# Kernel tuning notes

Hardware: AMD Instinct MI355X
Metric: run time of the kernel (lower is better)

Reference implementation:

```python
import jax, jax.numpy as jnp
import numpy as np

B, H, W, C = 32, 56, 56, 384
HEADS, WIN, SHIFT = 12, 7, 3
MLP_HID = 4 * C
N = WIN * WIN
EPS = 1e-5


def _rel_pos_index(win):
    ch, cw = np.meshgrid(np.arange(win), np.arange(win), indexing='ij')
    coords = np.stack([ch.ravel(), cw.ravel()])            # (2, N)
    rel = coords[:, :, None] - coords[:, None, :]          # (2, N, N)
    rel = rel.transpose(1, 2, 0).astype(np.int64)
    rel[:, :, 0] += win - 1
    rel[:, :, 1] += win - 1
    rel[:, :, 0] *= 2 * win - 1
    return rel.sum(-1)                                     # (N, N)


def _attn_mask(Hh, Ww, win, shift):
    img = np.zeros((Hh, Ww))
    cnt = 0
    slices = (slice(0, -win), slice(-win, -shift), slice(-shift, None))
    for hs in slices:
        for ws in slices:
            img[hs, ws] = cnt
            cnt += 1
    m = img.reshape(Hh // win, win, Ww // win, win).transpose(0, 2, 1, 3).reshape(-1, win * win)
    am = m[:, None, :] - m[:, :, None]
    return np.where(am != 0, -100.0, 0.0).astype(np.float32)  # (nW, N, N)


REL_IDX = jnp.asarray(_rel_pos_index(WIN))
ATTN_MASK = jnp.asarray(_attn_mask(H, W, WIN, SHIFT))


def setup_inputs() -> dict:
    key = jax.random.key(0)
    ks = jax.random.split(key, 16)
    s = 0.02
    return {
        'x': jax.random.normal(ks[0], (B, H * W, C), jnp.float32),
        'g1': jnp.ones((C,), jnp.float32),
        'b1': jnp.zeros((C,), jnp.float32),
        'qkv_w': jax.random.normal(ks[1], (3 * C, C), jnp.float32) * s,
        'qkv_b': jnp.zeros((3 * C,), jnp.float32),
        'rel_bias': jax.random.normal(ks[2], ((2 * WIN - 1) ** 2, HEADS), jnp.float32) * s,
        'proj_w': jax.random.normal(ks[3], (C, C), jnp.float32) * s,
        'proj_b': jnp.zeros((C,), jnp.float32),
        'g2': jnp.ones((C,), jnp.float32),
        'b2': jnp.zeros((C,), jnp.float32),
        'fc1_w': jax.random.normal(ks[4], (MLP_HID, C), jnp.float32) * s,
        'fc1_b': jnp.zeros((MLP_HID,), jnp.float32),
        'fc2_w': jax.random.normal(ks[5], (C, MLP_HID), jnp.float32) * s,
        'fc2_b': jnp.zeros((C,), jnp.float32),
    }


def _ln(x, g, b):
    m = x.mean(-1, keepdims=True)
    v = jnp.var(x, axis=-1, keepdims=True)
    return (x - m) * jax.lax.rsqrt(v + EPS) * g + b


def reference(x, g1, b1, qkv_w, qkv_b, rel_bias, proj_w, proj_b, g2, b2, fc1_w, fc1_b, fc2_w, fc2_b):
    Bz, L, Cc = x.shape
    hd = Cc // HEADS
    nWh = H // WIN
    shortcut = x

    h = _ln(x, g1, b1).reshape(Bz, H, W, Cc)
    h = jnp.roll(h, (-SHIFT, -SHIFT), axis=(1, 2))
    # window partition -> (Bz*nW, N, C)
    h = h.reshape(Bz, nWh, WIN, nWh, WIN, Cc).transpose(0, 1, 3, 2, 4, 5).reshape(-1, N, Cc)

    qkv = (h @ qkv_w.T + qkv_b).reshape(-1, N, 3, HEADS, hd).transpose(2, 0, 3, 1, 4)
    q, k, v = qkv[0] * (hd ** -0.5), qkv[1], qkv[2]
    attn = jnp.einsum('bhnd,bhmd->bhnm', q, k)  # (Bz*nW, heads, N, N)

    bias = rel_bias[REL_IDX.reshape(-1)].reshape(N, N, HEADS).transpose(2, 0, 1)
    attn = attn + bias[None]

    nW = ATTN_MASK.shape[0]
    attn = attn.reshape(Bz, nW, HEADS, N, N) + ATTN_MASK[None, :, None]
    attn = jax.nn.softmax(attn, axis=-1).reshape(-1, HEADS, N, N)

    out = jnp.einsum('bhnm,bhmd->bhnd', attn, v).transpose(0, 2, 1, 3).reshape(-1, N, Cc)
    out = out @ proj_w.T + proj_b
    # window reverse + unshift
    out = out.reshape(Bz, nWh, nWh, WIN, WIN, Cc).transpose(0, 1, 3, 2, 4, 5).reshape(Bz, H, W, Cc)
    out = jnp.roll(out, (SHIFT, SHIFT), axis=(1, 2)).reshape(Bz, L, Cc)

    x = shortcut + out
    h2 = _ln(x, g2, b2)
    h2 = jax.nn.gelu(h2 @ fc1_w.T + fc1_b, approximate=False)
    h2 = h2 @ fc2_w.T + fc2_b
    return x + h2
```

## Files before the change

kernel.cpp:

```cpp
#include <hip/hip_runtime.h>
#include <hip/hip_bf16.h>
#include <math.h>

#define B_      32
#define H_      56
#define W_      56
#define C_      384
#define HEADS_  12
#define WIN_    7
#define SHIFT_  3
#define NTOK_   49
#define HD_     32
#define T_      100352
#define MLP_    1536
#define TCH_    50176

typedef __bf16 bf16x8 __attribute__((ext_vector_type(8)));
typedef unsigned short u16x8 __attribute__((ext_vector_type(8)));
typedef float  f32x4  __attribute__((ext_vector_type(4)));

__device__ __forceinline__ float bf2f(unsigned short u) {
  union { unsigned int i; float f; } v; v.i = ((unsigned int)u) << 16; return v.f;
}
__device__ __forceinline__ unsigned short f2bf(float f) {
  union { float f; unsigned int i; } v; v.f = f;
  unsigned int x = v.i;
  return (unsigned short)((x + 0x7fffu + ((x >> 16) & 1u)) >> 16);
}
__device__ __forceinline__ float gelu_fast(float x) {
  const float t = 0.79788456f * x * (1.0f + 0.044715f * x * x);
  const float e = __expf(2.0f * t);
  const float th = 1.0f - 2.0f / (e + 1.0f);
  return 0.5f * x * (1.0f + th);
}
__device__ __forceinline__ void gload_lds16(const void* g, void* l) {
  __builtin_amdgcn_global_load_lds(
      (const __attribute__((address_space(1))) void*)g,
      (__attribute__((address_space(3))) void*)l, 16, 0, 0);
}
__device__ __forceinline__ bf16x8 ldg8(const unsigned short* p) {
  u16x8 v = *(const u16x8*)p;
  return __builtin_bit_cast(bf16x8, v);
}

__global__ __launch_bounds__(256)
void wconv_all_kernel(const float* __restrict__ s0, unsigned short* __restrict__ d0,
                      const float* __restrict__ s1, unsigned short* __restrict__ d1,
                      const float* __restrict__ s2, unsigned short* __restrict__ d2,
                      const float* __restrict__ s3, unsigned short* __restrict__ d3) {
  int b = blockIdx.x;
  const float* src; unsigned short* dst;
  if (b < 432)       { src = s0; dst = d0; }
  else if (b < 576)  { src = s1; dst = d1; b -= 432; }
  else if (b < 1152) { src = s2; dst = d2; b -= 576; }
  else               { src = s3; dst = d3; b -= 1152; }
  const int i = (b * 256 + threadIdx.x) * 4;
  const float4 v = *(const float4*)(src + i);
  ushort4 o;
  o.x = f2bf(v.x); o.y = f2bf(v.y); o.z = f2bf(v.z); o.w = f2bf(v.w);
  *(ushort4*)(dst + i) = o;
}

template<int REMAP>
__global__ __launch_bounds__(256)
void ln_kernel(const float* __restrict__ xin, const float* __restrict__ g,
               const float* __restrict__ bb, unsigned short* __restrict__ outbf) {
  const int m = blockIdx.x * 4 + (threadIdx.x >> 6);
  const int lane = threadIdx.x & 63;
  size_t src;
  if (REMAP) {
    int w = m / NTOK_, t = m - w * NTOK_;
    int bz = w >> 6, widx = w & 63;
    int wh = widx >> 3, ww = widx & 7;
    int ih = t / WIN_, iw = t - ih * WIN_;
    int gh = (wh * WIN_ + ih + SHIFT_) % H_;
    int gw = (ww * WIN_ + iw + SHIFT_) % W_;
    src = ((size_t)bz * (H_ * W_) + gh * W_ + gw) * C_;
  } else {
    src = (size_t)m * C_;
  }
  const float2* row2 = (const float2*)(xin + src);
  float2 v[3]; float s = 0.f, s2 = 0.f;
#pragma unroll
  for (int u = 0; u < 3; ++u) {
    v[u] = row2[lane + 64 * u];
    s  += v[u].x + v[u].y;
    s2 += v[u].x * v[u].x + v[u].y * v[u].y;
  }
#pragma unroll
  for (int off = 32; off; off >>= 1) {
    s  += __shfl_xor(s, off);
    s2 += __shfl_xor(s2, off);
  }
  const float mean = s * (1.0f / C_);
  const float var  = s2 * (1.0f / C_) - mean * mean;
  const float rstd = rsqrtf(var + 1e-5f);
  unsigned short* orow = outbf + (size_t)m * C_;
#pragma unroll
  for (int u = 0; u < 3; ++u) {
    const int c = (lane + 64 * u) * 2;
    ushort2 o;
    o.x = f2bf((v[u].x - mean) * rstd * g[c]     + bb[c]);
    o.y = f2bf((v[u].y - mean) * rstd * g[c + 1] + bb[c + 1]);
    *(ushort2*)(orow + c) = o;
  }
}

#define BM 256
#define BN 128
#define BKg 64

template<int EPI>
__global__ __launch_bounds__(512)
void mfma_gemm(const unsigned short* __restrict__ A,
               const unsigned short* __restrict__ Wb,
               const float* __restrict__ bias,
               void* __restrict__ outv,
               const float* __restrict__ resid,
               int M, int Nn, int K) {
  __shared__ unsigned short Al[BM * BKg];
  __shared__ unsigned short Bl[BN * BKg];
  const int t    = threadIdx.x;
  const int wid  = t >> 6;
  const int lane = t & 63;
  const int wr   = wid >> 1, wc = wid & 1;

  const unsigned int nb = gridDim.x * gridDim.y;
  const unsigned int lin = blockIdx.y * gridDim.x + blockIdx.x;
  const unsigned int q = nb >> 3, r = nb & 7;
  const unsigned int xcd = lin & 7, idx = lin >> 3;
  const unsigned int wg = (xcd < r ? xcd * (q + 1) : r * (q + 1) + (xcd - r) * q) + idx;
  const int m0 = (int)(wg / gridDim.x) * BM;
  const int n0 = (int)(wg % gridDim.x) * BN;

  f32x4 acc[4][4] = {};

  const int sr8    = lane >> 3;
  const int schunk = (lane & 7) ^ (sr8 & 7);
  const int fr  = lane & 15;
  const int fq  = lane >> 4;

  for (int k0 = 0; k0 < K; k0 += BKg) {
    __syncthreads();
#pragma unroll
    for (int i = 0; i < 4; ++i) {
      const int rr = i * 64 + wid * 8 + sr8;
      gload_lds16(A + (size_t)(m0 + rr) * K + k0 + schunk * 8,
                  (void*)(Al + (size_t)(i * 64 + wid * 8) * BKg));
    }
#pragma unroll
    for (int i = 0; i < 2; ++i) {
      const int rr = i * 64 + wid * 8 + sr8;
      gload_lds16(Wb + (size_t)(n0 + rr) * K + k0 + schunk * 8,
                  (void*)(Bl + (size_t)(i * 64 + wid * 8) * BKg));
    }
    __syncthreads();

#pragma unroll
    for (int kk = 0; kk < 2; ++kk) {
      bf16x8 af[4], bfr[4];
#pragma unroll
      for (int mi = 0; mi < 4; ++mi) {
        const int row = wr * 64 + mi * 16 + fr;
        const int ch  = (kk * 4 + fq) ^ (row & 7);
        af[mi] = *(const bf16x8*)(Al + (size_t)row * BKg + ch * 8);
      }
#pragma unroll
      for (int ni = 0; ni < 4; ++ni) {
        const int row = wc * 64 + ni * 16 + fr;
        const int ch  = (kk * 4 + fq) ^ (row & 7);
        bfr[ni] = *(const bf16x8*)(Bl + (size_t)row * BKg + ch * 8);
      }
#pragma unroll
      for (int mi = 0; mi < 4; ++mi)
#pragma unroll
        for (int ni = 0; ni < 4; ++ni)
          acc[mi][ni] = __builtin_amdgcn_mfma_f32_16x16x32_bf16(
              af[mi], bfr[ni], acc[mi][ni], 0, 0, 0);
    }
  }

  const int ecol  = fr;
  const int erow0 = fq * 4;
#pragma unroll
  for (int mi = 0; mi < 4; ++mi) {
#pragma unroll
    for (int r2 = 0; r2 < 4; ++r2) {
      const int m = m0 + wr * 64 + mi * 16 + erow0 + r2;
      size_t dstbase = 0;
      if (EPI == 2) {
        int w = m / NTOK_, tt = m - w * NTOK_;
        int bz = w >> 6, widx = w & 63;
        int wh = widx >> 3, ww = widx & 7;
        int ih = tt / WIN_, iw = tt - ih * WIN_;
        int gh = (wh * WIN_ + ih + SHIFT_) % H_;
        int gw = (ww * WIN_ + iw + SHIFT_) % W_;
        dstbase = ((size_t)bz * (H_ * W_) + gh * W_ + gw) * C_;
      }
#pragma unroll
      for (int ni = 0; ni < 4; ++ni) {
        const int n = n0 + wc * 64 + ni * 16 + ecol;
        float val = acc[mi][ni][r2] + bias[n];
        if (EPI == 0) {
          ((unsigned short*)outv)[(size_t)m * Nn + n] = f2bf(val);
        } else if (EPI == 1) {
          ((unsigned short*)outv)[(size_t)m * Nn + n] = f2bf(gelu_fast(val));
        } else if (EPI == 2) {
          ((float*)outv)[dstbase + n] = resid[dstbase + n] + val;
        } else {
          float* o = (float*)outv + (size_t)m * Nn + n;
          *o += val;
        }
      }
    }
  }
}

__global__ __launch_bounds__(64)
void bias_expand_kernel(const float* __restrict__ rel_bias,
                        float* __restrict__ biasx) {
  const int hi = blockIdx.x;
  const int head = hi / NTOK_, i = hi - head * NTOK_;
  const int j = threadIdx.x;
  float v = 0.f;
  if (j < NTOK_) {
    const int ih = i / 7, iw = i - ih * 7;
    const int jh = j / 7, jw = j - jh * 7;
    const int ridx = (ih - jh + 6) * 13 + (iw - jw + 6);
    v = rel_bias[ridx * HEADS_ + head];
  }
  biasx[(size_t)hi * 64 + j] = v;
}

#define AW 2
__global__ __launch_bounds__(64 * AW)
void attn_mfma_kernel(const unsigned short* __restrict__ qkv,
                      const float* __restrict__ biasx,
                      unsigned short* __restrict__ out) {
  __shared__ unsigned short sP[AW][64 * 72];
  __shared__ unsigned short sVT[AW][32 * 72];
  __shared__ float sRI[AW][64];
  const int wid  = threadIdx.x >> 6;
  const int lane = threadIdx.x & 63;
  const int task = blockIdx.x * AW + wid;
  const int w    = task / HEADS_;
  const int head = task - w * HEADS_;
  const int widx = w & 63;
  const int wh = widx >> 3, ww = widx & 7;
  const bool edge = (wh == 7) || (ww == 7);
  const int c  = lane & 15;
  const int fq = lane >> 4;
  unsigned short* Pl = sP[wid];
  unsigned short* Vl = sVT[wid];
  float* Ri = sRI[wid];
  const unsigned short* qw = qkv + (size_t)w * NTOK_ * (3 * C_);

  u16x8 vv[4];
#pragma unroll
  for (int p = 0; p < 4; ++p)
    vv[p] = *(const u16x8*)(qw + (size_t)(p * 16 + c) * (3 * C_) + 2 * C_ + head * HD_ + fq * 8);

  bf16x8 kf[4], qf[4];
#pragma unroll
  for (int nj = 0; nj < 4; ++nj)
    kf[nj] = ldg8(qw + (size_t)(nj * 16 + c) * (3 * C_) + C_ + head * HD_ + fq * 8);
#pragma unroll
  for (int qi = 0; qi < 4; ++qi)
    qf[qi] = ldg8(qw + (size_t)(qi * 16 + c) * (3 * C_) + head * HD_ + fq * 8);

  const f32x4 zero4 = {0.f, 0.f, 0.f, 0.f};
  f32x4 accT[4][4];
#pragma unroll
  for (int nj = 0; nj < 4; ++nj)
#pragma unroll
    for (int qi = 0; qi < 4; ++qi)
      accT[nj][qi] = __builtin_amdgcn_mfma_f32_16x16x32_bf16(kf[nj], qf[qi], zero4, 0, 0, 0);

#pragma unroll
  for (int p = 0; p < 4; ++p)
#pragma unroll
    for (int u = 0; u < 8; ++u)
      Vl[(fq * 8 + u) * 72 + p * 16 + c] = (unsigned short)vv[p][u];

  int lj16[16];
  unsigned jpad = 0;
#pragma unroll
  for (int tt = 0; tt < 16; ++tt) {
    const int j = (tt >> 2) * 16 + fq * 4 + (tt & 3);
    int lj = 0;
    if (j >= NTOK_) jpad |= (1u << tt);
    else if (edge) {
      const int jh = j / 7, jw2 = j - jh * 7;
      const int shj = wh * 7 + jh, swj = ww * 7 + jw2;
      lj = (shj < 49 ? 0 : (shj < 53 ? 1 : 2)) * 3 + (swj < 49 ? 0 : (swj < 53 ? 1 : 2));
    }
    lj16[tt] = lj;
  }

  const float* bh = biasx + (size_t)head * (NTOK_ * 64);
#pragma unroll
  for (int qi = 0; qi < 4; ++qi) {
    const int i  = qi * 16 + c;
    const int ic = i < NTOK_ ? i : 0;
    int li = 0;
    if (edge) {
      const int ih = ic / 7, iw2 = ic - ih * 7;
      const int shi = wh * 7 + ih, swi = ww * 7 + iw2;
      li = (shi < 49 ? 0 : (shi < 53 ? 1 : 2)) * 3 + (swi < 49 ? 0 : (swi < 53 ? 1 : 2));
    }
    float sv[16];
#pragma unroll
    for (int nj = 0; nj < 4; ++nj) {
      const float4 b4 = *(const float4*)(bh + ic * 64 + nj * 16 + fq * 4);
      const float* b4p = (const float*)&b4;
#pragma unroll
      for (int r = 0; r < 4; ++r) {
        const int tt = nj * 4 + r;
        float s = accT[nj][qi][r] * 0.17677669529663687f + b4p[r];
        if (edge && lj16[tt] != li) s -= 100.f;
        if (jpad & (1u << tt)) s = -1e30f;
        sv[tt] = s;
      }
    }
    float mx = sv[0];
#pragma unroll
    for (int tt = 1; tt < 16; ++tt) mx = fmaxf(mx, sv[tt]);
    mx = fmaxf(mx, __shfl_xor(mx, 16));
    mx = fmaxf(mx, __shfl_xor(mx, 32));
    float e[16]; float sm = 0.f;
#pragma unroll
    for (int tt = 0; tt < 16; ++tt) { e[tt] = __expf(sv[tt] - mx); sm += e[tt]; }
    sm += __shfl_xor(sm, 16);
    sm += __shfl_xor(sm, 32);
    if (fq == 0) Ri[i] = 1.0f / sm;
#pragma unroll
    for (int nj = 0; nj < 4; ++nj) {
      ushort4 pk;
      pk.x = f2bf(e[nj * 4 + 0]); pk.y = f2bf(e[nj * 4 + 1]);
      pk.z = f2bf(e[nj * 4 + 2]); pk.w = f2bf(e[nj * 4 + 3]);
      *(ushort4*)(Pl + (size_t)i * 72 + nj * 16 + fq * 4) = pk;
    }
  }

  f32x4 accO[4][2] = {};
#pragma unroll
  for (int kk = 0; kk < 2; ++kk) {
    bf16x8 ap[4], bv[2];
#pragma unroll
    for (int mi = 0; mi < 4; ++mi)
      ap[mi] = __builtin_bit_cast(bf16x8,
          *(const u16x8*)(Pl + (mi * 16 + c) * 72 + kk * 32 + fq * 8));
#pragma unroll
    for (int nd = 0; nd < 2; ++nd)
      bv[nd] = __builtin_bit_cast(bf16x8,
          *(const u16x8*)(Vl + (nd * 16 + c) * 72 + kk * 32 + fq * 8));
#pragma unroll
    for (int mi = 0; mi < 4; ++mi)
#pragma unroll
      for (int nd = 0; nd < 2; ++nd)
        accO[mi][nd] = __builtin_amdgcn_mfma_f32_16x16x32_bf16(ap[mi], bv[nd], accO[mi][nd], 0, 0, 0);
  }

#pragma unroll
  for (int mi = 0; mi < 4; ++mi)
#pragma unroll
    for (int r = 0; r < 4; ++r) {
      const int i = mi * 16 + fq * 4 + r;
      if (i < NTOK_) {
        const float inv = Ri[i];
#pragma unroll
        for (int nd = 0; nd < 2; ++nd)
          out[(size_t)(w * NTOK_ + i) * C_ + head * HD_ + nd * 16 + c] =
              f2bf(accO[mi][nd][r] * inv);
      }
    }
}

extern "C" void kernel_launch(void* const* d_in, const int* in_sizes, int n_in,
                              void* d_out, int out_size, void* d_ws, size_t ws_size,
                              hipStream_t stream) {
  const float* x        = (const float*)d_in[0];
  const float* g1       = (const float*)d_in[1];
  const float* b1       = (const float*)d_in[2];
  const float* qkv_w    = (const float*)d_in[3];
  const float* qkv_b    = (const float*)d_in[4];
  const float* rel_bias = (const float*)d_in[5];
  const float* proj_w   = (const float*)d_in[6];
  const float* proj_b   = (const float*)d_in[7];
  const float* g2       = (const float*)d_in[8];
  const float* b2       = (const float*)d_in[9];
  const float* fc1_w    = (const float*)d_in[10];
  const float* fc1_b    = (const float*)d_in[11];
  const float* fc2_w    = (const float*)d_in[12];
  const float* fc2_b    = (const float*)d_in[13];
  float* out = (float*)d_out;

  char* ws = (char*)d_ws;
  unsigned short* xw   = (unsigned short*)(ws);
  unsigned short* qkvb = (unsigned short*)(ws + 77070336);
  unsigned short* attn_out = xw;
  unsigned short* h2   = xw;
  unsigned short* hidc = qkvb;
  unsigned short* qkv_wb  = (unsigned short*)(ws + 308412416);
  unsigned short* proj_wb = (unsigned short*)(ws + 309297152);
  unsigned short* fc1_wb  = (unsigned short*)(ws + 309592064);
  unsigned short* fc2_wb  = (unsigned short*)(ws + 310771712);
  float*          biasx   = (float*)(ws + 311951360);

  wconv_all_kernel<<<dim3(1728), dim3(256), 0, stream>>>(
      qkv_w, qkv_wb, proj_w, proj_wb, fc1_w, fc1_wb, fc2_w, fc2_wb);
  bias_expand_kernel<<<dim3(HEADS_ * NTOK_), dim3(64), 0, stream>>>(rel_bias, biasx);

  ln_kernel<1><<<dim3(T_ / 4), dim3(256), 0, stream>>>(x, g1, b1, xw);

  mfma_gemm<0><<<dim3(1152 / BN, T_ / BM), dim3(512), 0, stream>>>(
      xw, qkv_wb, qkv_b, (void*)qkvb, nullptr, T_, 1152, 384);

  attn_mfma_kernel<<<dim3((T_ / NTOK_) * HEADS_ / AW), dim3(64 * AW), 0, stream>>>(
      qkvb, biasx, attn_out);

  mfma_gemm<2><<<dim3(384 / BN, T_ / BM), dim3(512), 0, stream>>>(
      attn_out, proj_wb, proj_b, (void*)out, x, T_, 384, 384);

  ln_kernel<0><<<dim3(T_ / 4), dim3(256), 0, stream>>>(out, g2, b2, h2);

  for (int chk = 0; chk < 2; ++chk) {
    const size_t row0 = (size_t)chk * TCH_;
    mfma_gemm<1><<<dim3(MLP_ / BN, TCH_ / BM), dim3(512), 0, stream>>>(
        h2 + row0 * C_, fc1_wb, fc1_b, (void*)hidc, nullptr, TCH_, MLP_, 384);
    mfma_gemm<3><<<dim3(384 / BN, TCH_ / BM), dim3(512), 0, stream>>>(
        hidc, fc2_wb, fc2_b, (void*)(out + row0 * C_), nullptr, TCH_, 384, MLP_);
  }
}
```

Before: 891.5 us.

## Merge prologue kernels, swizzle V LDS layout, raise MFMA priority

After: 883.6 us. About the same (-0.9%).

```diff
diff --git a/kernel.cpp b/kernel.cpp
--- a/kernel.cpp
+++ b/kernel.cpp
@@ -44,42 +44,87 @@
 }
 
 __global__ __launch_bounds__(256)
-void wconv_all_kernel(const float* __restrict__ s0, unsigned short* __restrict__ d0,
-                      const float* __restrict__ s1, unsigned short* __restrict__ d1,
-                      const float* __restrict__ s2, unsigned short* __restrict__ d2,
-                      const float* __restrict__ s3, unsigned short* __restrict__ d3) {
+void prologue_kernel(const float* __restrict__ s0, unsigned short* __restrict__ d0,
+                     const float* __restrict__ s1, unsigned short* __restrict__ d1,
+                     const float* __restrict__ s2, unsigned short* __restrict__ d2,
+                     const float* __restrict__ s3, unsigned short* __restrict__ d3,
+                     const float* __restrict__ rel_bias, float* __restrict__ biasx,
+                     const float* __restrict__ x, const float* __restrict__ g1,
+                     const float* __restrict__ b1, unsigned short* __restrict__ xw) {
   int b = blockIdx.x;
-  const float* src; unsigned short* dst;
-  if (b < 432)       { src = s0; dst = d0; }
-  else if (b < 576)  { src = s1; dst = d1; b -= 432; }
-  else if (b < 1152) { src = s2; dst = d2; b -= 576; }
-  else               { src = s3; dst = d3; b -= 1152; }
-  const int i = (b * 256 + threadIdx.x) * 4;
-  const float4 v = *(const float4*)(src + i);
-  ushort4 o;
-  o.x = f2bf(v.x); o.y = f2bf(v.y); o.z = f2bf(v.z); o.w = f2bf(v.w);
-  *(ushort4*)(dst + i) = o;
-}
-
-template<int REMAP>
-__global__ __launch_bounds__(256)
-void ln_kernel(const float* __restrict__ xin, const float* __restrict__ g,
-               const float* __restrict__ bb, unsigned short* __restrict__ outbf) {
-  const int m = blockIdx.x * 4 + (threadIdx.x >> 6);
-  const int lane = threadIdx.x & 63;
-  size_t src;
-  if (REMAP) {
+  if (b < 1728) {
+    const float* src; unsigned short* dst;
+    if (b < 432)       { src = s0; dst = d0; }
+    else if (b < 576)  { src = s1; dst = d1; b -= 432; }
+    else if (b < 1152) { src = s2; dst = d2; b -= 576; }
+    else               { src = s3; dst = d3; b -= 1152; }
+    const int i = (b * 256 + threadIdx.x) * 4;
+    const float4 v = *(const float4*)(src + i);
+    ushort4 o;
+    o.x = f2bf(v.x); o.y = f2bf(v.y); o.z = f2bf(v.z); o.w = f2bf(v.w);
+    *(ushort4*)(dst + i) = o;
+    return;
+  }
+  if (b < 1875) {
+    const int hi = (b - 1728) * 4 + (threadIdx.x >> 6);
+    const int j = threadIdx.x & 63;
+    if (hi < HEADS_ * NTOK_) {
+      const int head = hi / NTOK_, i = hi - head * NTOK_;
+      float v = 0.f;
+      if (j < NTOK_) {
+        const int ih = i / 7, iw = i - ih * 7;
+        const int jh = j / 7, jw = j - jh * 7;
+        const int ridx = (ih - jh + 6) * 13 + (iw - jw + 6);
+        v = rel_bias[ridx * HEADS_ + head];
+      }
+      biasx[(size_t)hi * 64 + j] = v;
+    }
+    return;
+  }
+  {
+    const int m = (b - 1875) * 4 + (threadIdx.x >> 6);
+    const int lane = threadIdx.x & 63;
     int w = m / NTOK_, t = m - w * NTOK_;
     int bz = w >> 6, widx = w & 63;
     int wh = widx >> 3, ww = widx & 7;
     int ih = t / WIN_, iw = t - ih * WIN_;
     int gh = (wh * WIN_ + ih + SHIFT_) % H_;
     int gw = (ww * WIN_ + iw + SHIFT_) % W_;
-    src = ((size_t)bz * (H_ * W_) + gh * W_ + gw) * C_;
-  } else {
-    src = (size_t)m * C_;
-  }
-  const float2* row2 = (const float2*)(xin + src);
+    const size_t srcoff = ((size_t)bz * (H_ * W_) + gh * W_ + gw) * C_;
+    const float2* row2 = (const float2*)(x + srcoff);
+    float2 v[3]; float sa = 0.f, sb = 0.f;
+#pragma unroll
+    for (int u = 0; u < 3; ++u) {
+      v[u] = row2[lane + 64 * u];
+      sa += v[u].x + v[u].y;
+      sb += v[u].x * v[u].x + v[u].y * v[u].y;
+    }
+#pragma unroll
+    for (int off = 32; off; off >>= 1) {
+      sa += __shfl_xor(sa, off);
+      sb += __shfl_xor(sb, off);
+    }
+    const float mean = sa * (1.0f / C_);
+    const float var  = sb * (1.0f / C_) - mean * mean;
+    const float rstd = rsqrtf(var + 1e-5f);
+    unsigned short* orow = xw + (size_t)m * C_;
+#pragma unroll
+    for (int u = 0; u < 3; ++u) {
+      const int cc = (lane + 64 * u) * 2;
+      ushort2 o;
+      o.x = f2bf((v[u].x - mean) * rstd * g1[cc]     + b1[cc]);
+      o.y = f2bf((v[u].y - mean) * rstd * g1[cc + 1] + b1[cc + 1]);
+      *(ushort2*)(orow + cc) = o;
+    }
+  }
+}
+
+__global__ __launch_bounds__(256)
+void ln_kernel(const float* __restrict__ xin, const float* __restrict__ g,
+               const float* __restrict__ bb, unsigned short* __restrict__ outbf) {
+  const int m = blockIdx.x * 4 + (threadIdx.x >> 6);
+  const int lane = threadIdx.x & 63;
+  const float2* row2 = (const float2*)(xin + (size_t)m * C_);
   float2 v[3]; float s = 0.f, s2 = 0.f;
 #pragma unroll
   for (int u = 0; u < 3; ++u) {
@@ -214,22 +259,6 @@
       }
     }
   }
-}
-
-__global__ __launch_bounds__(64)
-void bias_expand_kernel(const float* __restrict__ rel_bias,
-                        float* __restrict__ biasx) {
-  const int hi = blockIdx.x;
-  const int head = hi / NTOK_, i = hi - head * NTOK_;
-  const int j = threadIdx.x;
-  float v = 0.f;
-  if (j < NTOK_) {
-    const int ih = i / 7, iw = i - ih * 7;
-    const int jh = j / 7, jw = j - jh * 7;
-    const int ridx = (ih - jh + 6) * 13 + (iw - jw + 6);
-    v = rel_bias[ridx * HEADS_ + head];
-  }
-  biasx[(size_t)hi * 64 + j] = v;
 }
 
 #define AW 2
@@ -270,17 +299,22 @@
 
   const f32x4 zero4 = {0.f, 0.f, 0.f, 0.f};
   f32x4 accT[4][4];
+  __builtin_amdgcn_s_setprio(1);
 #pragma unroll
   for (int nj = 0; nj < 4; ++nj)
 #pragma unroll
     for (int qi = 0; qi < 4; ++qi)
       accT[nj][qi] = __builtin_amdgcn_mfma_f32_16x16x32_bf16(kf[nj], qf[qi], zero4, 0, 0, 0);
+  __builtin_amdgcn_s_setprio(0);
 
 #pragma unroll
   for (int p = 0; p < 4; ++p)
 #pragma unroll
-    for (int u = 0; u < 8; ++u)
-      Vl[(fq * 8 + u) * 72 + p * 16 + c] = (unsigned short)vv[p][u];
+    for (int u = 0; u < 8; ++u) {
+      const int d  = fq * 8 + u;
+      const int ch = (2 * p + (c >> 3)) ^ ((u + fq) & 7);
+      Vl[d * 72 + ch * 8 + (c & 7)] = (unsigned short)vv[p][u];
+    }
 
   int lj16[16];
   unsigned jpad = 0;
@@ -351,14 +385,18 @@
       ap[mi] = __builtin_bit_cast(bf16x8,
           *(const u16x8*)(Pl + (mi * 16 + c) * 72 + kk * 32 + fq * 8));
 #pragma unroll
-    for (int nd = 0; nd < 2; ++nd)
-      bv[nd] = __builtin_bit_cast(bf16x8,
-          *(const u16x8*)(Vl + (nd * 16 + c) * 72 + kk * 32 + fq * 8));
+    for (int nd = 0; nd < 2; ++nd) {
+      const int row = nd * 16 + c;
+      const int ch  = (kk * 4 + fq) ^ ((row + (row >> 3)) & 7);
+      bv[nd] = __builtin_bit_cast(bf16x8, *(const u16x8*)(Vl + row * 72 + ch * 8));
+    }
+    __builtin_amdgcn_s_setprio(1);
 #pragma unroll
     for (int mi = 0; mi < 4; ++mi)
 #pragma unroll
       for (int nd = 0; nd < 2; ++nd)
         accO[mi][nd] = __builtin_amdgcn_mfma_f32_16x16x32_bf16(ap[mi], bv[nd], accO[mi][nd], 0, 0, 0);
+    __builtin_amdgcn_s_setprio(0);
   }
 
 #pragma unroll
@@ -407,11 +445,9 @@
   unsigned short* fc2_wb  = (unsigned short*)(ws + 310771712);
   float*          biasx   = (float*)(ws + 311951360);
 
-  wconv_all_kernel<<<dim3(1728), dim3(256), 0, stream>>>(
-      qkv_w, qkv_wb, proj_w, proj_wb, fc1_w, fc1_wb, fc2_w, fc2_wb);
-  bias_expand_kernel<<<dim3(HEADS_ * NTOK_), dim3(64), 0, stream>>>(rel_bias, biasx);
-
-  ln_kernel<1><<<dim3(T_ / 4), dim3(256), 0, stream>>>(x, g1, b1, xw);
+  prologue_kernel<<<dim3(1728 + 147 + T_ / 4), dim3(256), 0, stream>>>(
+      qkv_w, qkv_wb, proj_w, proj_wb, fc1_w, fc1_wb, fc2_w, fc2_wb,
+      rel_bias, biasx, x, g1, b1, xw);
 
   mfma_gemm<0><<<dim3(1152 / BN, T_ / BM), dim3(512), 0, stream>>>(
       xw, qkv_wb, qkv_b, (void*)qkvb, nullptr, T_, 1152, 384);
@@ -422,7 +458,7 @@
   mfma_gemm<2><<<dim3(384 / BN, T_ / BM), dim3(512), 0, stream>>>(
       attn_out, proj_wb, proj_b, (void*)out, x, T_, 384, 384);
 
-  ln_kernel<0><<<dim3(T_ / 4), dim3(256), 0, stream>>>(out, g2, b2, h2);
+  ln_kernel<<<dim3(T_ / 4), dim3(256), 0, stream>>>(out, g2, b2, h2);
 
   for (int chk = 0; chk < 2; ++chk) {
     const size_t row0 = (size_t)chk * TCH_;
```
